# Kernel tuning notes

Hardware: AMD Instinct MI355X
Metric: run time of the kernel (lower is better)

The kernel has to match this reference:

```python
import jax, jax.numpy as jnp
import numpy as np

N_NODES = 100000
N_EDGES = 1600000
N_OBS, N_MID, N_ACT = 32, 64, 8


def setup_inputs() -> dict:
    key = jax.random.key(0)
    k1, k2, k3, k4, k5, k6 = jax.random.split(key, 6)
    x = jax.random.normal(k1, (N_NODES, N_OBS), dtype=jnp.float32)
    edge_index = jax.random.randint(k2, (2, N_EDGES), 0, N_NODES, dtype=jnp.int64)
    W1 = jax.random.normal(k3, (N_OBS, N_MID), dtype=jnp.float32) / np.sqrt(N_OBS)
    b1 = jax.random.normal(k4, (N_MID,), dtype=jnp.float32) * 0.01
    W2 = jax.random.normal(k5, (N_MID, N_ACT), dtype=jnp.float32) / np.sqrt(N_MID)
    b2 = jax.random.normal(k6, (N_ACT,), dtype=jnp.float32) * 0.01
    return {"x": x, "edge_index": edge_index, "W1": W1, "b1": b1, "W2": W2, "b2": b2}


def reference(x, edge_index, W1, b1, W2, b2):
    N = x.shape[0]
    # PyG GCNConv: add self-loops, symmetric deg^{-1/2} normalization,
    # linear transform before propagation, bias after aggregation.
    loops = jnp.arange(N, dtype=edge_index.dtype)
    src = jnp.concatenate([edge_index[0], loops])  # message sources (x_j)
    dst = jnp.concatenate([edge_index[1], loops])  # aggregation targets
    deg = jax.ops.segment_sum(jnp.ones_like(dst, dtype=x.dtype), dst, num_segments=N)
    dinv = jnp.where(deg > 0, jax.lax.rsqrt(deg), jnp.zeros_like(deg))
    norm = dinv[src] * dinv[dst]  # [E+N]
    h = x @ W1  # [N, n_mid]
    agg = jax.ops.segment_sum(h[src] * norm[:, None], dst, num_segments=N) + b1
    return jnp.tanh(agg) @ W2 + b2  # [N, n_action]
```

## Files before the change

### kernel.cpp

```cpp
#include <hip/hip_runtime.h>
#include <hip/hip_fp16.h>
#include <math.h>


#define NOBS 32
#define NMID 64
#define NACT 8
#define BSH 7
#define BNODES 128
#define CAP 4096
#define ARENA_B 16384
#define SPLIT_E 4096
#define NPW 4

typedef _Float16 half2v __attribute__((ext_vector_type(2)));

__device__ __forceinline__ bool edges_i64(const int* ei) {
    return (ei[1] | ei[3] | ei[5] | ei[7]) == 0;
}

__device__ __forceinline__ float fast_tanh(float x) {
    float t = __expf(2.f * x);
    return 1.f - 2.f * __builtin_amdgcn_rcpf(1.f + t);
}

__device__ __forceinline__ unsigned rlu(unsigned v, int lane) {
    return (unsigned)__builtin_amdgcn_readlane((int)v, lane);
}

__device__ __forceinline__ unsigned padd(unsigned a, unsigned b) {
    __half2 r = __hadd2(__builtin_bit_cast(__half2, a),
                        __builtin_bit_cast(__half2, b));
    return __builtin_bit_cast(unsigned, r);
}

__device__ __forceinline__ float fdot2u(unsigned a, unsigned b, float c) {
    return __builtin_amdgcn_fdot2(__builtin_bit_cast(half2v, a),
                                  __builtin_bit_cast(half2v, b), c, false);
}

__global__ __launch_bounds__(256) void k_split(
        const int* __restrict__ ei, int* __restrict__ gcnt,
        unsigned int* __restrict__ arena, long long e, int nbuckets) {
    __shared__ int sbuf[SPLIT_E];
    __shared__ int offs[1024];
    __shared__ int cur[1024];
    __shared__ int tsum[256];
    const int tid = threadIdx.x;
    int eb[16];
    int bk[16];

    for (int b = tid; b < 1024; b += 256) cur[b] = 0;
    __syncthreads();

    const long long base = (long long)blockIdx.x * SPLIT_E;
    const bool i64 = edges_i64(ei);
    const long long* e64 = (const long long*)ei;
#pragma unroll
    for (int j = 0; j < 8; ++j) {
        const int kk = j * 512 + tid * 2;
        const long long ge = base + kk;
        const bool v0 = ge < e, v1 = ge + 1 < e;
        int s0 = 0, d0 = 0, s1 = 0, d1 = 0;
        if (v1) {
            if (i64) {
                ulonglong2 sp = *(const ulonglong2*)(e64 + ge);
                ulonglong2 dp = *(const ulonglong2*)(e64 + e + ge);
                s0 = (int)sp.x; s1 = (int)sp.y; d0 = (int)dp.x; d1 = (int)dp.y;
            } else {
                int2 sp = *(const int2*)(ei + ge);
                int2 dp = *(const int2*)(ei + e + ge);
                s0 = sp.x; s1 = sp.y; d0 = dp.x; d1 = dp.y;
            }
        } else if (v0) {
            if (i64) { s0 = (int)e64[ge]; d0 = (int)e64[e + ge]; }
            else     { s0 = ei[ge];       d0 = ei[e + ge]; }
        }
        eb[2 * j]     = s0 | ((d0 & (BNODES - 1)) << 20);
        bk[2 * j]     = v0 ? (d0 >> BSH) : -1;
        eb[2 * j + 1] = s1 | ((d1 & (BNODES - 1)) << 20);
        bk[2 * j + 1] = v1 ? (d1 >> BSH) : -1;
        if (v0) atomicAdd(&cur[d0 >> BSH], 1);
        if (v1) atomicAdd(&cur[d1 >> BSH], 1);
    }
    __syncthreads();

    const int t4 = tid * 4;
    int s0 = cur[t4], s1 = cur[t4 + 1], s2 = cur[t4 + 2], s3 = cur[t4 + 3];
    int my = s0 + s1 + s2 + s3;
    tsum[tid] = my;
    __syncthreads();
    for (int off = 1; off < 256; off <<= 1) {
        int t = (tid >= off) ? tsum[tid - off] : 0;
        __syncthreads();
        tsum[tid] += t;
        __syncthreads();
    }
    int ex = tsum[tid] - my;
    offs[t4] = ex;
    offs[t4 + 1] = ex + s0;
    offs[t4 + 2] = ex + s0 + s1;
    offs[t4 + 3] = ex + s0 + s1 + s2;
    __syncthreads();
    for (int b = tid; b < 1024; b += 256) cur[b] = offs[b];
    __syncthreads();

#pragma unroll
    for (int j = 0; j < 16; ++j) {
        if (bk[j] >= 0) {
            int slot = atomicAdd(&cur[bk[j]], 1);
            sbuf[slot] = eb[j];
        }
    }
    __syncthreads();

    for (int b = tid; b < nbuckets; b += 256) {
        int beg = offs[b];
        int len = cur[b] - beg;
        if (len <= 0) continue;
        int g = atomicAdd(&gcnt[b], len);
        if (g >= CAP) continue;
        if (g + len > CAP) len = CAP - g;
        unsigned int* dst = arena + (size_t)b * CAP + g;
        for (int j = 0; j < len; ++j) dst[j] = (unsigned int)sbuf[beg + j];
    }
}

__global__ __launch_bounds__(256) void k_sort(
        const int* __restrict__ gcnt, unsigned int* __restrict__ arena,
        const float* __restrict__ x, uint2* __restrict__ pkd,
        __half2* __restrict__ y2, int n) {
    __shared__ unsigned int sbuf[CAP];
    __shared__ unsigned int obuf[CAP];
    __shared__ int hist[BNODES];
    __shared__ int offs[BNODES];
    __shared__ int cur[BNODES];
    __shared__ float rinv[BNODES];
    const int b = blockIdx.x, tid = threadIdx.x;
    const int count = min(gcnt[b], CAP);
    unsigned int* ent = arena + (size_t)b * CAP;

    if (tid < BNODES) hist[tid] = 0;
    __syncthreads();
    for (int p = tid; p < count; p += 256) {
        unsigned int v = ent[p];
        sbuf[p] = v;
        atomicAdd(&hist[v >> 20], 1);
    }
    __syncthreads();
    if (tid < BNODES) offs[tid] = hist[tid];
    __syncthreads();
    for (int off = 1; off < BNODES; off <<= 1) {
        int t = 0;
        if (tid < BNODES && tid >= off) t = offs[tid - off];
        __syncthreads();
        if (tid < BNODES) offs[tid] += t;
        __syncthreads();
    }
    if (tid < BNODES) {
        int ex = offs[tid] - hist[tid];
        cur[tid] = ex;
        float r = rsqrtf((float)(hist[tid] + 1));
        rinv[tid] = r;
        int node = b * BNODES + tid;
        if (node < n) {
            uint2 pd;
            pd.x = (unsigned int)(b * CAP + ex) | ((unsigned int)hist[tid] << 22);
            pd.y = __float_as_uint(r);
            pkd[node] = pd;
        }
    }
    __syncthreads();
    for (int p = tid; p < count; p += 256) {
        unsigned int v = sbuf[p];
        int pos = atomicAdd(&cur[v >> 20], 1);
        obuf[pos] = v;
    }
    for (int idx = tid; idx < BNODES * 16; idx += 256) {
        int node = b * BNODES + (idx >> 4);
        if (node >= n) break;
        float r = rinv[idx >> 4];
        float2 v = ((const float2*)x)[(size_t)node * 16 + (idx & 15)];
        y2[(size_t)node * 16 + (idx & 15)] = __floats2half2_rn(v.x * r, v.y * r);
    }
    __syncthreads();
    for (int p = tid; p < count; p += 256) ent[p] = obuf[p];
}

__global__ __launch_bounds__(256, 4) void k_fused(
        const unsigned int* __restrict__ arena, const uint2* __restrict__ pkd,
        const __half2* __restrict__ y2,
        const float* __restrict__ W1, const float* __restrict__ b1,
        const float* __restrict__ W2, const float* __restrict__ b2,
        float* __restrict__ out, int n) {
    __shared__ float sT[4][NMID];
    const int tid = threadIdx.x;
    const int wid = tid >> 6;
    const int lane = tid & 63;
    const int g = lane >> 3, l = lane & 7;
    const int jg = lane >> 3, k = lane & 7;
    const char* y2c = (const char*)y2;

    unsigned w1h[16];
#pragma unroll
    for (int c2 = 0; c2 < 16; ++c2) {
        __half2 h = __floats2half2_rn(W1[(2 * c2) * NMID + lane],
                                      W1[(2 * c2 + 1) * NMID + lane]);
        w1h[c2] = __builtin_bit_cast(unsigned, h);
    }
    float w2row[8];
#pragma unroll
    for (int jj = 0; jj < 8; ++jj) w2row[jj] = W2[(jg * 8 + jj) * NACT + k];
    const float b1v = b1[lane];
    const float b2v = b2[k];

    const int nodeBase = blockIdx.x * (4 * NPW) + wid * NPW;

    uint2 pd[NPW];
    uint2 sv[NPW];
#pragma unroll
    for (int nn = 0; nn < NPW; ++nn) {
        const int node = nodeBase + nn;
        const bool valid = node < n;
        pd[nn] = valid ? pkd[node] : make_uint2(0u, 0u);
        sv[nn] = make_uint2(0u, 0u);
        if (valid && g == 0) {
            unsigned off = ((unsigned)node << 6) | ((unsigned)l << 3);
            sv[nn] = *(const uint2*)(y2c + off);
        }
    }
    unsigned int en[4];
    {
        const unsigned beg0 = pd[0].x & 0x3FFFFF;
#pragma unroll
        for (int w = 0; w < 4; ++w) en[w] = arena[beg0 + g + 8 * w];
    }

#pragma unroll
    for (int nn = 0; nn < NPW; ++nn) {
        const int node = nodeBase + nn;
        const bool valid = node < n;

        const unsigned beg = pd[nn].x & 0x3FFFFF;
        const int cnt = valid ? (int)(pd[nn].x >> 22) : 0;
        const float din = __uint_as_float(pd[nn].y);

        bool ok[4];
        uint2 v[4];
#pragma unroll
        for (int w = 0; w < 4; ++w) {
            ok[w] = g + 8 * w < cnt;
            const unsigned idx = ok[w] ? (en[w] & 0xFFFFF) : 0u;
            const unsigned off = (idx << 6) | ((unsigned)l << 3);
            v[w] = *(const uint2*)(y2c + off);
        }

        if (nn + 1 < NPW) {
            const unsigned begN = pd[nn + 1].x & 0x3FFFFF;
#pragma unroll
            for (int w = 0; w < 4; ++w) en[w] = arena[begN + g + 8 * w];
        }

        unsigned acc0 = sv[nn].x, acc1 = sv[nn].y;
#pragma unroll
        for (int w = 0; w < 4; ++w) {
            if (!ok[w]) { v[w].x = 0u; v[w].y = 0u; }
            acc0 = padd(acc0, v[w].x);
            acc1 = padd(acc1, v[w].y);
        }
        if (cnt > 32) {
            for (int i = 32 + g; i < cnt; i += 8) {
                unsigned ee = arena[beg + i];
                unsigned off = ((ee & 0xFFFFF) << 6) | ((unsigned)l << 3);
                uint2 vv = *(const uint2*)(y2c + off);
                acc0 = padd(acc0, vv.x);
                acc1 = padd(acc1, vv.y);
            }
        }
#pragma unroll
        for (int off = 8; off < 64; off <<= 1) {
            acc0 = padd(acc0, (unsigned)__shfl_xor((int)acc0, off));
            acc1 = padd(acc1, (unsigned)__shfl_xor((int)acc1, off));
        }

        float sA = 0.f, sB = 0.f;
#pragma unroll
        for (int s = 0; s < 8; ++s) {
            sA = fdot2u(rlu(acc0, s), w1h[2 * s + 0], sA);
            sB = fdot2u(rlu(acc1, s), w1h[2 * s + 1], sB);
        }
        const float m = fmaf(din, sA + sB, b1v);
        sT[wid][lane] = fast_tanh(m);
        asm volatile("s_waitcnt lgkmcnt(0)" ::: "memory");
        __builtin_amdgcn_sched_barrier(0);

        float o = 0.f;
#pragma unroll
        for (int jj = 0; jj < 8; ++jj)
            o = fmaf(sT[wid][jg * 8 + jj], w2row[jj], o);
        o += __shfl_xor(o, 8);
        o += __shfl_xor(o, 16);
        o += __shfl_xor(o, 32);
        if (valid && jg == 0)
            out[(size_t)node * NACT + k] = o + b2v;
    }
}

extern "C" void kernel_launch(void* const* d_in, const int* in_sizes, int n_in,
                              void* d_out, int out_size, void* d_ws, size_t ws_size,
                              hipStream_t stream) {
    const float* x  = (const float*)d_in[0];
    const int*   ei = (const int*)d_in[1];
    const float* W1 = (const float*)d_in[2];
    const float* b1 = (const float*)d_in[3];
    const float* W2 = (const float*)d_in[4];
    const float* b2 = (const float*)d_in[5];
    float* out = (float*)d_out;

    const int n = in_sizes[0] / NOBS;
    const long long e = in_sizes[1] / 2;
    const int B = (n + BNODES - 1) >> BSH;

    char* ws = (char*)d_ws;
    int*          gcnt  = (int*)ws;
    unsigned int* arena = (unsigned int*)(ws + 4096);
    uint2*        pkd   = (uint2*)(ws + 4096 + (size_t)B * ARENA_B);
    __half2*      y2    = (__half2*)(ws + 4096 + (size_t)B * ARENA_B + (size_t)n * 8);

    hipMemsetAsync(gcnt, 0, 4096, stream);
    int nsb = (int)((e + SPLIT_E - 1) / SPLIT_E);
    k_split<<<nsb, 256, 0, stream>>>(ei, gcnt, arena, e, B);
    k_sort<<<B, 256, 0, stream>>>(gcnt, arena, x, pkd, y2, n);
    const int npb = 4 * NPW;
    k_fused<<<(n + npb - 1) / npb, 256, 0, stream>>>(arena, pkd, y2,
                                                     W1, b1, W2, b2, out, n);
}
```

Measured before the change: 84.07 us.

## Remap gather lanes and use DPP reductions with fewer nodes per wave

```diff
diff --git a/kernel.cpp b/kernel.cpp
--- a/kernel.cpp
+++ b/kernel.cpp
@@ -11,7 +11,7 @@
 #define CAP 4096
 #define ARENA_B 16384
 #define SPLIT_E 4096
-#define NPW 4
+#define NPW 2
 
 typedef _Float16 half2v __attribute__((ext_vector_type(2)));
 
@@ -37,6 +37,20 @@
 __device__ __forceinline__ float fdot2u(unsigned a, unsigned b, float c) {
     return __builtin_amdgcn_fdot2(__builtin_bit_cast(half2v, a),
                                   __builtin_bit_cast(half2v, b), c, false);
+}
+
+__device__ __forceinline__ unsigned padd_dpp_xor1(unsigned a) {
+    return padd(a, (unsigned)__builtin_amdgcn_mov_dpp((int)a, 0xB1, 0xF, 0xF, true));
+}
+__device__ __forceinline__ unsigned padd_dpp_xor2(unsigned a) {
+    return padd(a, (unsigned)__builtin_amdgcn_mov_dpp((int)a, 0x4E, 0xF, 0xF, true));
+}
+__device__ __forceinline__ unsigned padd_swz_xor4(unsigned a) {
+    return padd(a, (unsigned)__builtin_amdgcn_ds_swizzle((int)a, 0x101F));
+}
+__device__ __forceinline__ float fadd_dpp_xor8(float a) {
+    int r = __builtin_amdgcn_mov_dpp(__float_as_int(a), 0x128, 0xF, 0xF, true);
+    return a + __int_as_float(r);
 }
 
 __global__ __launch_bounds__(256) void k_split(
@@ -197,8 +211,9 @@
     const int tid = threadIdx.x;
     const int wid = tid >> 6;
     const int lane = tid & 63;
-    const int g = lane >> 3, l = lane & 7;
+    const int g = lane & 7, l = lane >> 3;
     const int jg = lane >> 3, k = lane & 7;
+    const unsigned lByte = (unsigned)l << 3;
     const char* y2c = (const char*)y2;
 
     unsigned w1h[16];
@@ -225,15 +240,15 @@
         pd[nn] = valid ? pkd[node] : make_uint2(0u, 0u);
         sv[nn] = make_uint2(0u, 0u);
         if (valid && g == 0) {
-            unsigned off = ((unsigned)node << 6) | ((unsigned)l << 3);
+            unsigned off = ((unsigned)node << 6) | lByte;
             sv[nn] = *(const uint2*)(y2c + off);
         }
     }
-    unsigned int en[4];
+    unsigned en0[4], en1[4];
     {
         const unsigned beg0 = pd[0].x & 0x3FFFFF;
 #pragma unroll
-        for (int w = 0; w < 4; ++w) en[w] = arena[beg0 + g + 8 * w];
+        for (int w = 0; w < 4; ++w) en0[w] = arena[beg0 + g + 8 * w];
     }
 
 #pragma unroll
@@ -244,61 +259,79 @@
         const unsigned beg = pd[nn].x & 0x3FFFFF;
         const int cnt = valid ? (int)(pd[nn].x >> 22) : 0;
         const float din = __uint_as_float(pd[nn].y);
-
-        bool ok[4];
-        uint2 v[4];
-#pragma unroll
-        for (int w = 0; w < 4; ++w) {
-            ok[w] = g + 8 * w < cnt;
-            const unsigned idx = ok[w] ? (en[w] & 0xFFFFF) : 0u;
-            const unsigned off = (idx << 6) | ((unsigned)l << 3);
-            v[w] = *(const uint2*)(y2c + off);
+        const unsigned* en = (nn == 0) ? en0 : en1;
+
+        const bool big = cnt > 16;
+        uint2 v0, v1, v2, v3;
+        const bool ok0 = g < cnt, ok1 = g + 8 < cnt;
+        {
+            const unsigned i0 = ok0 ? (en[0] & 0xFFFFF) : 0u;
+            const unsigned i1 = ok1 ? (en[1] & 0xFFFFF) : 0u;
+            v0 = *(const uint2*)(y2c + ((i0 << 6) | lByte));
+            v1 = *(const uint2*)(y2c + ((i1 << 6) | lByte));
+        }
+        bool ok2 = false, ok3 = false;
+        if (big) {
+            ok2 = g + 16 < cnt; ok3 = g + 24 < cnt;
+            const unsigned i2 = ok2 ? (en[2] & 0xFFFFF) : 0u;
+            const unsigned i3 = ok3 ? (en[3] & 0xFFFFF) : 0u;
+            v2 = *(const uint2*)(y2c + ((i2 << 6) | lByte));
+            v3 = *(const uint2*)(y2c + ((i3 << 6) | lByte));
         }
 
         if (nn + 1 < NPW) {
             const unsigned begN = pd[nn + 1].x & 0x3FFFFF;
 #pragma unroll
-            for (int w = 0; w < 4; ++w) en[w] = arena[begN + g + 8 * w];
+            for (int w = 0; w < 4; ++w) en1[w] = arena[begN + g + 8 * w];
         }
 
         unsigned acc0 = sv[nn].x, acc1 = sv[nn].y;
-#pragma unroll
-        for (int w = 0; w < 4; ++w) {
-            if (!ok[w]) { v[w].x = 0u; v[w].y = 0u; }
-            acc0 = padd(acc0, v[w].x);
-            acc1 = padd(acc1, v[w].y);
-        }
-        if (cnt > 32) {
-            for (int i = 32 + g; i < cnt; i += 8) {
-                unsigned ee = arena[beg + i];
-                unsigned off = ((ee & 0xFFFFF) << 6) | ((unsigned)l << 3);
-                uint2 vv = *(const uint2*)(y2c + off);
-                acc0 = padd(acc0, vv.x);
-                acc1 = padd(acc1, vv.y);
+        if (!ok0) { v0.x = 0u; v0.y = 0u; }
+        if (!ok1) { v1.x = 0u; v1.y = 0u; }
+        acc0 = padd(acc0, padd(v0.x, v1.x));
+        acc1 = padd(acc1, padd(v0.y, v1.y));
+        if (big) {
+            if (!ok2) { v2.x = 0u; v2.y = 0u; }
+            if (!ok3) { v3.x = 0u; v3.y = 0u; }
+            acc0 = padd(acc0, padd(v2.x, v3.x));
+            acc1 = padd(acc1, padd(v2.y, v3.y));
+            if (cnt > 32) {
+                for (int i = 32 + g; i < cnt; i += 8) {
+                    unsigned ee = arena[beg + i];
+                    unsigned off = ((ee & 0xFFFFF) << 6) | lByte;
+                    uint2 vv = *(const uint2*)(y2c + off);
+                    acc0 = padd(acc0, vv.x);
+                    acc1 = padd(acc1, vv.y);
+                }
             }
         }
-#pragma unroll
-        for (int off = 8; off < 64; off <<= 1) {
-            acc0 = padd(acc0, (unsigned)__shfl_xor((int)acc0, off));
-            acc1 = padd(acc1, (unsigned)__shfl_xor((int)acc1, off));
-        }
+
+        acc0 = padd_dpp_xor1(acc0);  acc1 = padd_dpp_xor1(acc1);
+        acc0 = padd_dpp_xor2(acc0);  acc1 = padd_dpp_xor2(acc1);
+        acc0 = padd_swz_xor4(acc0);  acc1 = padd_swz_xor4(acc1);
 
         float sA = 0.f, sB = 0.f;
 #pragma unroll
         for (int s = 0; s < 8; ++s) {
-            sA = fdot2u(rlu(acc0, s), w1h[2 * s + 0], sA);
-            sB = fdot2u(rlu(acc1, s), w1h[2 * s + 1], sB);
+            sA = fdot2u(rlu(acc0, 8 * s), w1h[2 * s + 0], sA);
+            sB = fdot2u(rlu(acc1, 8 * s), w1h[2 * s + 1], sB);
         }
         const float m = fmaf(din, sA + sB, b1v);
         sT[wid][lane] = fast_tanh(m);
         asm volatile("s_waitcnt lgkmcnt(0)" ::: "memory");
         __builtin_amdgcn_sched_barrier(0);
 
-        float o = 0.f;
-#pragma unroll
-        for (int jj = 0; jj < 8; ++jj)
-            o = fmaf(sT[wid][jg * 8 + jj], w2row[jj], o);
-        o += __shfl_xor(o, 8);
+        const float4* tp = (const float4*)(&sT[wid][jg * 8]);
+        float4 ta = tp[0], tb = tp[1];
+        float o = ta.x * w2row[0];
+        o = fmaf(ta.y, w2row[1], o);
+        o = fmaf(ta.z, w2row[2], o);
+        o = fmaf(ta.w, w2row[3], o);
+        o = fmaf(tb.x, w2row[4], o);
+        o = fmaf(tb.y, w2row[5], o);
+        o = fmaf(tb.z, w2row[6], o);
+        o = fmaf(tb.w, w2row[7], o);
+        o = fadd_dpp_xor8(o);
         o += __shfl_xor(o, 16);
         o += __shfl_xor(o, 32);
         if (valid && jg == 0)
```

After: 94.09 us. 11.9% more time.
